# Kernel optimization log

Hardware: AMD Instinct MI355X
Metric: run time of the kernel (lower is better)

## Reference

```python
import jax, jax.numpy as jnp
import numpy as np

B, L, D = 2, 256, 256


def setup_inputs() -> dict:
    key = jax.random.key(0)
    k1, k2, k3, k4 = jax.random.split(key, 4)
    x = jax.random.normal(k1, (B, L, D), dtype=jnp.float32)
    # nn.Linear(dim, 2*dim, bias=False): weight (2*dim, dim), out = x @ W.T
    W_a = jax.random.normal(k2, (2 * D, D), dtype=jnp.float32) / np.sqrt(D).astype(np.float32)
    # last_hidden_init: complex (dim,) parameter, split into real/imag floats
    h0_real = jax.random.normal(k3, (D,), dtype=jnp.float32)
    h0_imag = jax.random.normal(k4, (D,), dtype=jnp.float32)
    return {"x": x, "W_a": W_a, "h0_real": h0_real, "h0_imag": h0_imag}


def reference(x, W_a, h0_real, h0_imag):
    b, l, d = x.shape
    # a = view_as_complex(linear_a(x).float().view(b, l, d, 2))
    raw = (x.astype(jnp.float32) @ W_a.T).reshape(b, l, d, 2)
    re, im = raw[..., 0], raw[..., 1]
    mag2 = re * re + im * im                       # |a|^2
    a = jax.lax.complex(re, im) * (jax.lax.rsqrt(mag2) * jnp.exp(-mag2))
    a_ln = jnp.log(a)                              # (b, l, d) complex
    a_ln = jnp.transpose(a_ln, (0, 2, 1))          # (b, d, l)

    ii = jnp.arange(l)[:, None]
    kk = jnp.arange(l)[None, :]
    # a_ln_tri[b,d,i,k] = a_ln[b,d,k] if k >= i else 0 (== .triu())
    tri = jnp.where(kk >= ii, a_ln[:, :, None, :], 0.0)   # (b, d, l, l)
    # FFT causal conv with ones(len,len) row == cumulative sum along k
    cum = jnp.cumsum(tri, axis=-1)
    # c[b,d,i,k] = exp(sum_{j=i}^{k} a_ln_j) for k>=i, 1 at k=i-1, 0 below (.triu(-1))
    c = jnp.where(kk >= ii - 1, jnp.exp(cum), 0.0)         # (b, d, l, l)

    xT = jnp.transpose(x.astype(jnp.complex64), (0, 2, 1))  # (b, d, l)
    x_hat = jnp.roll(xT, 1, axis=2)                          # x_hat[k] = x[k-1]
    h0 = jax.lax.complex(h0_real, h0_imag)                   # (d,)
    x_hat = x_hat.at[:, :, 0].set(jnp.broadcast_to(h0, (b, d)))
    # x_mat does not depend on i, so (x_mat * c).sum(3) == einsum over k
    h = jnp.einsum('bdik,bdk->bdi', c, x_hat)
    h = h.at[:, :, -1].add(xT[:, :, -1])
    return jnp.transpose(h.real, (0, 2, 1)).astype(x.dtype)  # (b, l, d)
```

## Files before the change

### kernel.cpp

```cpp
#include <hip/hip_runtime.h>
#include <hip/hip_bf16.h>


constexpr int B = 2, L = 256, D = 256, K = 256;
constexpr int TL = 32;
constexpr int TD = 16;
constexpr int PADW = 260;

__global__ __launch_bounds__(256) void gemm_a_kernel(
    const float* __restrict__ x,
    const float* __restrict__ W,
    float2* __restrict__ aT)
{
    const int dt = blockIdx.x;
    const int lt = blockIdx.y;
    const int b  = blockIdx.z;
    const int t  = threadIdx.x;
    const int l0 = lt * TL;
    const int d0 = dt * TD;

    __shared__ float xs[TL][PADW];
    __shared__ float ws[2 * TD][PADW];

    {
        const float4* src = (const float4*)(x + (size_t)(b * L + l0) * K);
#pragma unroll
        for (int j = 0; j < 8; ++j) {
            const int g = j * 256 + t;
            const int row = g >> 6, c4 = g & 63;
            *(float4*)&xs[row][c4 * 4] = src[g];
        }
    }
    {
        const float4* src = (const float4*)(W + (size_t)(2 * d0) * K);
#pragma unroll
        for (int j = 0; j < 8; ++j) {
            const int g = j * 256 + t;
            const int row = g >> 6, c4 = g & 63;
            *(float4*)&ws[row][(c4 ^ ((row >> 1) & 7)) * 4] = src[g];
        }
    }
    __syncthreads();

    const int dgrp = t & 15;
    const int lgrp = t >> 4;
    const int sw   = dgrp & 7;

    float rr0 = 0.f, ii0 = 0.f, rr1 = 0.f, ii1 = 0.f;
#pragma unroll 8
    for (int k4 = 0; k4 < K / 4; ++k4) {
        const int kc = (k4 ^ sw) * 4;
        const float4 w0  = *(const float4*)&ws[2 * dgrp][kc];
        const float4 w1  = *(const float4*)&ws[2 * dgrp + 1][kc];
        const float4 xv0 = *(const float4*)&xs[2 * lgrp][k4 * 4];
        const float4 xv1 = *(const float4*)&xs[2 * lgrp + 1][k4 * 4];
        rr0 += xv0.x * w0.x + xv0.y * w0.y + xv0.z * w0.z + xv0.w * w0.w;
        ii0 += xv0.x * w1.x + xv0.y * w1.y + xv0.z * w1.z + xv0.w * w1.w;
        rr1 += xv1.x * w0.x + xv1.y * w0.y + xv1.z * w0.z + xv1.w * w0.w;
        ii1 += xv1.x * w1.x + xv1.y * w1.y + xv1.z * w1.z + xv1.w * w1.w;
    }

    const int d = d0 + dgrp;
#pragma unroll
    for (int i = 0; i < 2; ++i) {
        const float re = i ? rr1 : rr0, im = i ? ii1 : ii0;
        const float m2 = re * re + im * im;
        const float s  = rsqrtf(m2) * expf(-m2);
        aT[((size_t)b * D + d) * L + (l0 + 2 * lgrp + i)] = make_float2(re * s, im * s);
    }
}

__global__ __launch_bounds__(256) void scan_h_kernel(
    const float* __restrict__ x,
    const float2* __restrict__ aT,
    const float* __restrict__ h0r,
    const float* __restrict__ h0i,
    float* __restrict__ out)
{
    const int b = blockIdx.x >> 8;
    const int d = blockIdx.x & 255;
    const int i = threadIdx.x;

    __shared__ float4 Ms[L];
    __shared__ float  xcol[L];

    const size_t colbase = (size_t)b * L * D + d;

    const float2 ai = aT[((size_t)b * D + d) * L + i];
    xcol[i] = x[colbase + (size_t)i * D];
    __syncthreads();

    float xr, xi;
    if (i == 0) { xr = h0r[d]; xi = h0i[d]; }
    else        { xr = xcol[i - 1]; xi = 0.f; }

    float Ar = ai.x, Ai = ai.y;
    float Br = ai.x * xr - ai.y * xi;
    float Bi = ai.x * xi + ai.y * xr;

#pragma unroll
    for (int o = 1; o < L; o <<= 1) {
        Ms[i] = make_float4(Ar, Ai, Br, Bi);
        __syncthreads();
        if (i + o < L) {
            const float4 n = Ms[i + o];
            const float nAr = Ar * n.x - Ai * n.y;
            const float nAi = Ar * n.y + Ai * n.x;
            const float nBr = Ar * n.z - Ai * n.w + Br;
            const float nBi = Ar * n.w + Ai * n.z + Bi;
            Ar = nAr; Ai = nAi; Br = nBr; Bi = nBi;
        }
        __syncthreads();
    }

    float o_val = Br;
    if (i >= 2)      o_val += xcol[i - 2];
    else if (i == 1) o_val += h0r[d];
    if (i == L - 1)  o_val += xcol[L - 1];
    out[colbase + (size_t)i * D] = o_val;
}

extern "C" void kernel_launch(void* const* d_in, const int* in_sizes, int n_in,
                              void* d_out, int out_size, void* d_ws, size_t ws_size,
                              hipStream_t stream) {
    const float* x    = (const float*)d_in[0];
    const float* W_a  = (const float*)d_in[1];
    const float* h0r  = (const float*)d_in[2];
    const float* h0i  = (const float*)d_in[3];
    float* out = (float*)d_out;
    float2* aT = (float2*)d_ws;

    gemm_a_kernel<<<dim3(D / TD, L / TL, B), dim3(256), 0, stream>>>(x, W_a, aT);
    scan_h_kernel<<<dim3(B * D), dim3(256), 0, stream>>>(x, aT, h0r, h0i, out);
}
```

Measured before the change: 69.25 us.

## Retile GEMM to stage W in LDS and read x rows directly from global

Changes the GEMM tiling so each block holds 64 d-columns of W (128 rows) in shared memory, while each wavefront reads its two x rows straight from global memory as wave-uniform broadcast loads. This removes the x staging into LDS and cuts x-tile redundancy, so each block covers 8 sequence positions instead of 32. In exchange, the W load per block is four times larger and uses about 133 KB of LDS, which limits occupancy to one block per CU. The x loads now depend on global/L1 latency inside the inner loop.

```diff
diff --git a/kernel.cpp b/kernel.cpp
--- a/kernel.cpp
+++ b/kernel.cpp
@@ -3,8 +3,6 @@
 
 
 constexpr int B = 2, L = 256, D = 256, K = 256;
-constexpr int TL = 32;
-constexpr int TD = 16;
 constexpr int PADW = 260;
 
 __global__ __launch_bounds__(256) void gemm_a_kernel(
@@ -12,29 +10,18 @@
     const float* __restrict__ W,
     float2* __restrict__ aT)
 {
-    const int dt = blockIdx.x;
+    const int dq = blockIdx.x;
     const int lt = blockIdx.y;
     const int b  = blockIdx.z;
     const int t  = threadIdx.x;
-    const int l0 = lt * TL;
-    const int d0 = dt * TD;
+    const int d0 = dq * 64;
 
-    __shared__ float xs[TL][PADW];
-    __shared__ float ws[2 * TD][PADW];
+    __shared__ float ws[128][PADW];
 
-    {
-        const float4* src = (const float4*)(x + (size_t)(b * L + l0) * K);
-#pragma unroll
-        for (int j = 0; j < 8; ++j) {
-            const int g = j * 256 + t;
-            const int row = g >> 6, c4 = g & 63;
-            *(float4*)&xs[row][c4 * 4] = src[g];
-        }
-    }
     {
         const float4* src = (const float4*)(W + (size_t)(2 * d0) * K);
 #pragma unroll
-        for (int j = 0; j < 8; ++j) {
+        for (int j = 0; j < 32; ++j) {
             const int g = j * 256 + t;
             const int row = g >> 6, c4 = g & 63;
             *(float4*)&ws[row][(c4 ^ ((row >> 1) & 7)) * 4] = src[g];
@@ -42,31 +29,35 @@
     }
     __syncthreads();
 
-    const int dgrp = t & 15;
-    const int lgrp = t >> 4;
-    const int sw   = dgrp & 7;
+    const int dl = t & 63;
+    const int wv = __builtin_amdgcn_readfirstlane(t >> 6);
+    const int l0 = lt * 8 + wv * 2;
+    const int sw = dl & 7;
 
-    float rr0 = 0.f, ii0 = 0.f, rr1 = 0.f, ii1 = 0.f;
-#pragma unroll 8
+    const float* xr0 = x + (size_t)(b * L + l0) * K;
+    const float* xr1 = xr0 + K;
+
+    float re0 = 0.f, im0 = 0.f, re1 = 0.f, im1 = 0.f;
+#pragma unroll 4
     for (int k4 = 0; k4 < K / 4; ++k4) {
         const int kc = (k4 ^ sw) * 4;
-        const float4 w0  = *(const float4*)&ws[2 * dgrp][kc];
-        const float4 w1  = *(const float4*)&ws[2 * dgrp + 1][kc];
-        const float4 xv0 = *(const float4*)&xs[2 * lgrp][k4 * 4];
-        const float4 xv1 = *(const float4*)&xs[2 * lgrp + 1][k4 * 4];
-        rr0 += xv0.x * w0.x + xv0.y * w0.y + xv0.z * w0.z + xv0.w * w0.w;
-        ii0 += xv0.x * w1.x + xv0.y * w1.y + xv0.z * w1.z + xv0.w * w1.w;
-        rr1 += xv1.x * w0.x + xv1.y * w0.y + xv1.z * w0.z + xv1.w * w0.w;
-        ii1 += xv1.x * w1.x + xv1.y * w1.y + xv1.z * w1.z + xv1.w * w1.w;
+        const float4 w0 = *(const float4*)&ws[2 * dl][kc];
+        const float4 w1 = *(const float4*)&ws[2 * dl + 1][kc];
+        const float4 x0 = *(const float4*)(xr0 + k4 * 4);
+        const float4 x1 = *(const float4*)(xr1 + k4 * 4);
+        re0 += x0.x * w0.x + x0.y * w0.y + x0.z * w0.z + x0.w * w0.w;
+        im0 += x0.x * w1.x + x0.y * w1.y + x0.z * w1.z + x0.w * w1.w;
+        re1 += x1.x * w0.x + x1.y * w0.y + x1.z * w0.z + x1.w * w0.w;
+        im1 += x1.x * w1.x + x1.y * w1.y + x1.z * w1.z + x1.w * w1.w;
     }
 
-    const int d = d0 + dgrp;
+    const int d = d0 + dl;
 #pragma unroll
     for (int i = 0; i < 2; ++i) {
-        const float re = i ? rr1 : rr0, im = i ? ii1 : ii0;
+        const float re = i ? re1 : re0, im = i ? im1 : im0;
         const float m2 = re * re + im * im;
         const float s  = rsqrtf(m2) * expf(-m2);
-        aT[((size_t)b * D + d) * L + (l0 + 2 * lgrp + i)] = make_float2(re * s, im * s);
+        aT[((size_t)b * D + d) * L + (l0 + i)] = make_float2(re * s, im * s);
     }
 }
 
@@ -130,6 +121,6 @@
     float* out = (float*)d_out;
     float2* aT = (float2*)d_ws;
 
-    gemm_a_kernel<<<dim3(D / TD, L / TL, B), dim3(256), 0, stream>>>(x, W_a, aT);
+    gemm_a_kernel<<<dim3(D / 64, L / 8, B), dim3(256), 0, stream>>>(x, W_a, aT);
     scan_h_kernel<<<dim3(B * D), dim3(256), 0, stream>>>(x, aT, h0r, h0i, out);
 }
```

New measurement: 73.88 us. +6.7%, slower.
